# Kernel tuning notes

Hardware: AMD Instinct MI355X
Metric: run time of the kernel (lower is better)

Reference implementation:

```python
import jax, jax.numpy as jnp
import numpy as np

B, S, CIN = 4, 512, 512
H, I, N, R, K, L = 768, 1536, 16, 48, 4, 4  # mamba-130m dims, 4 layers
EPS = 1e-5


def setup_inputs() -> dict:
    key = jax.random.key(0)
    ks = jax.random.split(key, 8)
    g = lambda k, shape, s=0.02: jax.random.normal(k, shape, jnp.float32) * s
    x = jax.random.normal(ks[0], (B, S, CIN), jnp.float32)
    # HF Mamba init: A = 1..N repeated over channels, stored as log
    A_log = jnp.log(jnp.broadcast_to(jnp.arange(1, N + 1, dtype=jnp.float32), (L, I, N)))
    dt_bias = jnp.full((L, I), float(np.log(np.expm1(0.01))), jnp.float32)  # softplus^-1(0.01)
    return {
        'x': x,
        'W_in': g(ks[1], (CIN, H)), 'b_in': jnp.zeros((H,), jnp.float32),
        'norm_w': jnp.ones((L, H), jnp.float32),
        'in_proj_w': g(ks[2], (L, H, 2 * I)),
        'conv_w': g(ks[3], (L, I, K), 0.2), 'conv_b': jnp.zeros((L, I), jnp.float32),
        'x_proj_w': g(ks[4], (L, I, R + 2 * N)),
        'dt_proj_w': g(ks[5], (L, R, I), 0.05), 'dt_proj_b': dt_bias,
        'A_log': A_log, 'D': jnp.ones((L, I), jnp.float32),
        'out_proj_w': g(ks[6], (L, I, H)),
        'norm_f_w': jnp.ones((H,), jnp.float32),
    }


def _rmsnorm(x, w):
    return x * jax.lax.rsqrt(jnp.mean(x * x, -1, keepdims=True) + EPS) * w


def _selective_scan(xc, dt, A, Bm, Cm, Dp):
    # xc, dt: [B,S,I]; A: [I,N]; Bm, Cm: [B,S,N]; Dp: [I]
    dA = jnp.exp(dt[..., None] * A)                    # [B,S,I,N]
    dBx = (dt * xc)[..., None] * Bm[:, :, None, :]     # [B,S,I,N]

    def step(h, ins):
        dA_t, dBx_t, C_t = ins
        h = dA_t * h + dBx_t                           # [B,I,N]
        return h, jnp.einsum('bin,bn->bi', h, C_t)

    h0 = jnp.zeros((xc.shape[0], I, N), xc.dtype)
    _, ys = jax.lax.scan(step, h0, (jnp.swapaxes(dA, 0, 1),
                                    jnp.swapaxes(dBx, 0, 1),
                                    jnp.swapaxes(Cm, 0, 1)))
    return jnp.swapaxes(ys, 0, 1) + xc * Dp            # [B,S,I]


def _block(h, nw, ipw, cw, cb, xpw, dpw, dpb, Al, Dp, opw):
    res = h
    u = _rmsnorm(h, nw)
    xz = u @ ipw                                       # [B,S,2I]
    xc, z = jnp.split(xz, 2, axis=-1)
    xc_t = jnp.swapaxes(xc, 1, 2)                      # [B,I,S]
    xc_t = jax.lax.conv_general_dilated(
        xc_t, cw[:, None, :], (1,), [(K - 1, 0)],
        dimension_numbers=('NCH', 'OIH', 'NCH'), feature_group_count=I)
    xc = jax.nn.silu(jnp.swapaxes(xc_t, 1, 2) + cb)    # causal depthwise conv + SiLU
    dbc = xc @ xpw                                     # [B,S,R+2N]
    dt, Bm, Cm = dbc[..., :R], dbc[..., R:R + N], dbc[..., R + N:]
    dt = jax.nn.softplus(dt @ dpw + dpb)               # [B,S,I]
    y = _selective_scan(xc, dt, -jnp.exp(Al), Bm, Cm, Dp)
    y = y * jax.nn.silu(z)
    return res + y @ opw


def reference(x, W_in, b_in, norm_w, in_proj_w, conv_w, conv_b, x_proj_w,
              dt_proj_w, dt_proj_b, A_log, D, out_proj_w, norm_f_w):
    h = x @ W_in + b_in                                # project_in
    for l in range(L):
        h = _block(h, norm_w[l], in_proj_w[l], conv_w[l], conv_b[l], x_proj_w[l],
                   dt_proj_w[l], dt_proj_b[l], A_log[l], D[l], out_proj_w[l])
    return _rmsnorm(h, norm_f_w)                       # final norm_f; dropout = identity (eval)
```

## Files before the change

kernel.cpp:

```cpp
#include <hip/hip_runtime.h>
#include <cmath>

#define B_    4
#define S_    512
#define CIN_  512
#define H_    768
#define I_    1536
#define N_    16
#define R_    48
#define K_    4
#define L_    4
#define EPS_  1e-5f
#define MROWS (B_ * S_)
#define C_    16
#define T_    (S_ / C_)

typedef __attribute__((ext_vector_type(8))) short bf16x8;
typedef __attribute__((ext_vector_type(4))) float f32x4;
typedef __attribute__((ext_vector_type(4))) short s16x4;

__device__ __forceinline__ float fexpf(float x) { return __expf(x); }
__device__ __forceinline__ float siluf(float x) { return x / (1.f + __expf(-x)); }
__device__ __forceinline__ float softplusf(float x) { return x > 20.f ? x : __logf(1.f + __expf(x)); }
__device__ __forceinline__ short f2bf(float f) {
    union { float f; unsigned u; } v; v.f = f;
    unsigned r = v.u + 0x7fff + ((v.u >> 16) & 1);
    return (short)(r >> 16);
}
__device__ __forceinline__ float bf2f(short s) {
    union { float f; unsigned u; } v;
    v.u = ((unsigned)(unsigned short)s) << 16;
    return v.f;
}

#define GLOAD16(g, l) __builtin_amdgcn_global_load_lds( \
    (const __attribute__((address_space(1))) void*)(g), \
    (__attribute__((address_space(3))) void*)(l), 16, 0, 0)

#define ASTRIDE (64 * 64)
#define BSTRIDE (128 * 64)

__global__ __launch_bounds__(256) void gemm_mfma(
    const short* __restrict__ A, const short* __restrict__ Bt,
    const float* __restrict__ bias, void* __restrict__ Cv_,
    int M, int N, int Kd, int lda, int ldb, int ldc, int ep)
{
    __shared__ __align__(16) short Asl[2 * ASTRIDE];
    __shared__ __align__(16) short Bsl[2 * BSTRIDE];
    const int tid = threadIdx.x;
    const int ln  = tid & 63;
    const int wv  = tid >> 6;
    const int wm  = wv >> 1, wn = wv & 1;
    const int nwg  = gridDim.x * gridDim.y;
    const int orig = blockIdx.y * gridDim.x + blockIdx.x;
    const int qq   = nwg >> 3;
    const int swz  = (orig & 7) * qq + (orig >> 3);
    const int bx   = swz % gridDim.x;
    const int by   = swz / gridDim.x;
    const int row0 = by * 64;
    const int col0 = bx * 128;
    const int nz   = gridDim.z;
    const int kchunk = Kd / nz;
    const int kbeg   = blockIdx.z * kchunk;
    float* C = (float*)Cv_;
    short* Cb = (short*)Cv_;

    f32x4 acc[2][4];
    #pragma unroll
    for (int i = 0; i < 2; ++i)
        #pragma unroll
        for (int j = 0; j < 4; ++j) acc[i][j] = (f32x4){0.f, 0.f, 0.f, 0.f};

    const int ca0 = tid, ca1 = tid + 256;
    const int rowa0 = ca0 >> 3, kpa0 = (ca0 & 7) ^ (rowa0 & 7);
    const int rowa1 = ca1 >> 3, kpa1 = (ca1 & 7) ^ (rowa1 & 7);
    const short* ga0 = A + (size_t)(row0 + rowa0) * lda + kpa0 * 8;
    const short* ga1 = A + (size_t)(row0 + rowa1) * lda + kpa1 * 8;
    const int cb0 = tid, cb1 = tid + 256, cb2 = tid + 512, cb3 = tid + 768;
    const int rowb0 = cb0 >> 3, kpb0 = (cb0 & 7) ^ (rowb0 & 7);
    const int rowb1 = cb1 >> 3, kpb1 = (cb1 & 7) ^ (rowb1 & 7);
    const int rowb2 = cb2 >> 3, kpb2 = (cb2 & 7) ^ (rowb2 & 7);
    const int rowb3 = cb3 >> 3, kpb3 = (cb3 & 7) ^ (rowb3 & 7);
    const short* gb0 = Bt + (size_t)(col0 + rowb0) * ldb + kpb0 * 8;
    const short* gb1 = Bt + (size_t)(col0 + rowb1) * ldb + kpb1 * 8;
    const short* gb2 = Bt + (size_t)(col0 + rowb2) * ldb + kpb2 * 8;
    const short* gb3 = Bt + (size_t)(col0 + rowb3) * ldb + kpb3 * 8;
    short* la0 = &Asl[(wv * 64) * 8];
    short* la1 = &Asl[(256 + wv * 64) * 8];
    short* lb0 = &Bsl[(wv * 64) * 8];
    short* lb1 = &Bsl[(256 + wv * 64) * 8];
    short* lb2 = &Bsl[(512 + wv * 64) * 8];
    short* lb3 = &Bsl[(768 + wv * 64) * 8];

    const int lrow = ln & 15;
    const int kq0  = ln >> 4;
    const int nt   = kchunk / 64;

#define ISSUE_TILE(T, BI) do {                      \
    const int kI_ = kbeg + (T) * 64;                \
    GLOAD16(ga0 + kI_, la0 + (BI) * ASTRIDE);       \
    GLOAD16(ga1 + kI_, la1 + (BI) * ASTRIDE);       \
    GLOAD16(gb0 + kI_, lb0 + (BI) * BSTRIDE);       \
    GLOAD16(gb1 + kI_, lb1 + (BI) * BSTRIDE);       \
    GLOAD16(gb2 + kI_, lb2 + (BI) * BSTRIDE);       \
    GLOAD16(gb3 + kI_, lb3 + (BI) * BSTRIDE);       \
} while (0)

    ISSUE_TILE(0, 0);
    __syncthreads();

    for (int t = 0; t < nt; ++t) {
        const int cur = t & 1;
        const int nxt = cur ^ 1;
        if (t + 1 < nt) ISSUE_TILE(t + 1, nxt);
        const short* Ac = &Asl[cur * ASTRIDE];
        const short* Bc = &Bsl[cur * BSTRIDE];
        #pragma unroll
        for (int kk = 0; kk < 2; ++kk) {
            const int kq = kk * 4 + kq0;
            bf16x8 af[2], bfr[4];
            #pragma unroll
            for (int fm = 0; fm < 2; ++fm) {
                int r = wm * 32 + fm * 16 + lrow;
                int slot = r * 8 + (kq ^ (r & 7));
                af[fm] = *(const bf16x8*)&Ac[slot * 8];
            }
            #pragma unroll
            for (int fn = 0; fn < 4; ++fn) {
                int r = wn * 64 + fn * 16 + lrow;
                int slot = r * 8 + (kq ^ (r & 7));
                bfr[fn] = *(const bf16x8*)&Bc[slot * 8];
            }
            #pragma unroll
            for (int fm = 0; fm < 2; ++fm)
                #pragma unroll
                for (int fn = 0; fn < 4; ++fn)
                    acc[fm][fn] = __builtin_amdgcn_mfma_f32_16x16x32_bf16(
                        af[fm], bfr[fn], acc[fm][fn], 0, 0, 0);
        }
        __syncthreads();
    }
#undef ISSUE_TILE

    const int erow = (ln >> 4) * 4;
    const int ecol = ln & 15;
    const size_t zoff = (size_t)blockIdx.z * M * ldc;
    #pragma unroll
    for (int fm = 0; fm < 2; ++fm) {
        #pragma unroll
        for (int fn = 0; fn < 4; ++fn) {
            int gn = col0 + wn * 64 + fn * 16 + ecol;
            if (gn >= N) continue;
            #pragma unroll
            for (int r = 0; r < 4; ++r) {
                int gm = row0 + wm * 32 + fm * 16 + erow + r;
                float v = acc[fm][fn][r];
                size_t o = (size_t)gm * ldc + gn;
                if (nz > 1) { C[zoff + o] = v; continue; }
                if (ep == 4)      { Cb[o] = f2bf(v); continue; }
                if (ep == 5)      { Cb[o] = f2bf(softplusf(v + bias[gn])); continue; }
                if (ep == 1)      v += bias[gn];
                else if (ep == 2) v  = softplusf(v + bias[gn]);
                else if (ep == 3) v += C[o];
                C[o] = v;
            }
        }
    }
}

__global__ __launch_bounds__(256) void reduce_parts(
    const float* __restrict__ part, float* __restrict__ C,
    const float* __restrict__ bias, short* __restrict__ d48,
    int total, int ldc, int nz, int mode)
{
    int idx = blockIdx.x * 256 + threadIdx.x;
    if (idx >= total) return;
    size_t strideZ = (size_t)total;
    float s = 0.f;
    for (int z = 0; z < nz; ++z) s += part[idx + z * strideZ];
    if (mode == 1)      s += bias[idx % ldc];
    else if (mode == 2) s += C[idx];
    C[idx] = s;
    if (d48) {
        int row = idx / ldc, col = idx - row * ldc;
        if (col < 48)       d48[(size_t)row * 64 + col] = f2bf(s);
        else if (col >= 64) d48[(size_t)row * 64 + (col - 16)] = 0;
    }
}

__global__ __launch_bounds__(256) void reduce_h_rms(
    const float* __restrict__ part, float* __restrict__ h,
    const float* __restrict__ bias, const float* __restrict__ w,
    short* __restrict__ ubf, float* __restrict__ outf, int nz, int mode)
{
    const int row = blockIdx.x;
    const int t   = threadIdx.x;
    const size_t base = (size_t)row * H_;
    const size_t strideZ = (size_t)MROWS * H_;
    float v0, v1, v2;
    {
        size_t i0 = base + t, i1 = i0 + 256, i2 = i0 + 512;
        float s0 = 0.f, s1 = 0.f, s2 = 0.f;
        for (int z = 0; z < nz; ++z) {
            size_t zo = (size_t)z * strideZ;
            s0 += part[i0 + zo]; s1 += part[i1 + zo]; s2 += part[i2 + zo];
        }
        if (mode == 0) {
            s0 += bias[t]; s1 += bias[t + 256]; s2 += bias[t + 512];
        } else {
            s0 += h[i0]; s1 += h[i1]; s2 += h[i2];
        }
        h[i0] = s0; h[i1] = s1; h[i2] = s2;
        v0 = s0; v1 = s1; v2 = s2;
    }
    float ss = v0 * v0 + v1 * v1 + v2 * v2;
    #pragma unroll
    for (int off = 32; off > 0; off >>= 1) ss += __shfl_down(ss, off, 64);
    __shared__ float red[4];
    __shared__ float stot;
    if ((t & 63) == 0) red[t >> 6] = ss;
    __syncthreads();
    if (t == 0) stot = red[0] + red[1] + red[2] + red[3];
    __syncthreads();
    const float scale = rsqrtf(stot / (float)H_ + EPS_);
    if (mode == 2) {
        outf[base + t]       = v0 * scale * w[t];
        outf[base + t + 256] = v1 * scale * w[t + 256];
        outf[base + t + 512] = v2 * scale * w[t + 512];
    } else {
        ubf[base + t]       = f2bf(v0 * scale * w[t]);
        ubf[base + t + 256] = f2bf(v1 * scale * w[t + 256]);
        ubf[base + t + 512] = f2bf(v2 * scale * w[t + 512]);
    }
}

__global__ __launch_bounds__(256) void wtrans(
    const float* __restrict__ in0, short* __restrict__ out0,
    int Kd, int Nn, int Kpad, int Npad, size_t inStride, size_t outStride)
{
    const float* in  = in0  + blockIdx.z * inStride;
    short*       out = out0 + blockIdx.z * outStride;
    __shared__ float t[32][33];
    const int n0 = blockIdx.x * 32, k0 = blockIdx.y * 32;
    const int tx = threadIdx.x, ty = threadIdx.y;
    #pragma unroll
    for (int j = 0; j < 32; j += 8) {
        int k = k0 + ty + j, n = n0 + tx;
        t[ty + j][tx] = (k < Kd && n < Nn) ? in[(size_t)k * Nn + n] : 0.f;
    }
    __syncthreads();
    #pragma unroll
    for (int j = 0; j < 32; j += 8) {
        int np = n0 + ty + j, kp = k0 + tx;
        if (np < Npad && kp < Kpad) out[(size_t)np * Kpad + kp] = f2bf(t[tx][ty + j]);
    }
}

__global__ __launch_bounds__(256) void cast_bf16(
    const float* __restrict__ in, short* __restrict__ out, int n4)
{
    int i = blockIdx.x * 256 + threadIdx.x;
    if (i >= n4) return;
    float4 v = ((const float4*)in)[i];
    out[i * 4 + 0] = f2bf(v.x); out[i * 4 + 1] = f2bf(v.y);
    out[i * 4 + 2] = f2bf(v.z); out[i * 4 + 3] = f2bf(v.w);
}

__global__ __launch_bounds__(256) void conv_silu_kernel(
    const short* __restrict__ xzbf, const float* __restrict__ cw,
    const float* __restrict__ cb, short* __restrict__ xcb16)
{
    int idx = blockIdx.x * 256 + threadIdx.x;
    if (idx >= (MROWS / 4) * (I_ / 4)) return;
    const int i4 = (idx % (I_ / 4)) * 4;
    const int g4 = idx / (I_ / 4);
    const int s0 = (g4 % (S_ / 4)) * 4;
    const int b  = g4 / (S_ / 4);
    const short* base = xzbf + (size_t)b * S_ * (2 * I_) + i4;

    float4 wch[4];
    #pragma unroll
    for (int c = 0; c < 4; ++c) wch[c] = *(const float4*)&cw[(i4 + c) * K_];
    const float4 bv = *(const float4*)&cb[i4];

    float xv[7][4];
    #pragma unroll
    for (int r = 0; r < 7; ++r) {
        int row = s0 - 3 + r;
        if (row >= 0) {
            s16x4 t = *(const s16x4*)&base[(size_t)row * (2 * I_)];
            xv[r][0] = bf2f(t[0]); xv[r][1] = bf2f(t[1]);
            xv[r][2] = bf2f(t[2]); xv[r][3] = bf2f(t[3]);
        } else {
            xv[r][0] = 0.f; xv[r][1] = 0.f; xv[r][2] = 0.f; xv[r][3] = 0.f;
        }
    }

    #pragma unroll
    for (int j = 0; j < 4; ++j) {
        float a0 = bv.x, a1 = bv.y, a2 = bv.z, a3 = bv.w;
        #pragma unroll
        for (int k = 0; k < K_; ++k) {
            const float w0 = ((const float*)&wch[0])[k];
            const float w1 = ((const float*)&wch[1])[k];
            const float w2 = ((const float*)&wch[2])[k];
            const float w3 = ((const float*)&wch[3])[k];
            a0 = fmaf(w0, xv[j + k][0], a0);
            a1 = fmaf(w1, xv[j + k][1], a1);
            a2 = fmaf(w2, xv[j + k][2], a2);
            a3 = fmaf(w3, xv[j + k][3], a3);
        }
        s16x4 r;
        r[0] = f2bf(siluf(a0)); r[1] = f2bf(siluf(a1));
        r[2] = f2bf(siluf(a2)); r[3] = f2bf(siluf(a3));
        *(s16x4*)&xcb16[((size_t)b * S_ + s0 + j) * I_ + i4] = r;
    }
}

__global__ __launch_bounds__(256) void scan_pass1(
    const short* __restrict__ xcbf, const short* __restrict__ dtbf,
    const float* __restrict__ dbc, const float* __restrict__ A_log,
    short* __restrict__ P, short* __restrict__ hend)
{
    __shared__ float Bsh[T_][16];
    __shared__ float dtsh[T_][64];
    __shared__ float xcsh[T_][64];
    const int tid = threadIdx.x;
    const int lc  = tid >> 2;
    const int sub = tid & 3;
    const int ib  = blockIdx.x % (I_ / 64);
    const int c   = (blockIdx.x / (I_ / 64)) % C_;
    const int b   = blockIdx.x / ((I_ / 64) * C_);
    const int i   = ib * 64 + lc;
    const int s0  = c * T_;

    for (int idx = tid; idx < T_ * 4; idx += 256) {
        int row = idx >> 2, q = idx & 3;
        *(float4*)&Bsh[row][q * 4] =
            *(const float4*)&dbc[((size_t)b * S_ + s0 + row) * 80 + R_ + q * 4];
    }
    for (int idx = tid; idx < T_ * 16; idx += 256) {
        int row = idx >> 4, q = idx & 15;
        size_t g = ((size_t)b * S_ + s0 + row) * I_ + ib * 64 + q * 4;
        s16x4 dv = *(const s16x4*)&dtbf[g];
        dtsh[row][q * 4 + 0] = bf2f(dv[0]);
        dtsh[row][q * 4 + 1] = bf2f(dv[1]);
        dtsh[row][q * 4 + 2] = bf2f(dv[2]);
        dtsh[row][q * 4 + 3] = bf2f(dv[3]);
        s16x4 xv = *(const s16x4*)&xcbf[g];
        xcsh[row][q * 4 + 0] = bf2f(xv[0]);
        xcsh[row][q * 4 + 1] = bf2f(xv[1]);
        xcsh[row][q * 4 + 2] = bf2f(xv[2]);
        xcsh[row][q * 4 + 3] = bf2f(xv[3]);
    }

    float4 al = *(const float4*)&A_log[i * N_ + sub * 4];
    float a[4] = {-fexpf(al.x), -fexpf(al.y), -fexpf(al.z), -fexpf(al.w)};
    float h[4] = {0.f, 0.f, 0.f, 0.f}, p[4] = {1.f, 1.f, 1.f, 1.f};
    __syncthreads();

    #pragma unroll 4
    for (int s = 0; s < T_; ++s) {
        float dtv = dtsh[s][lc];
        float xcv = xcsh[s][lc];
        float4 Bv = *(const float4*)&Bsh[s][sub * 4];
        float dx = dtv * xcv;
        #pragma unroll
        for (int j = 0; j < 4; ++j) {
            float dA = fexpf(dtv * a[j]);
            float Bj = (j == 0) ? Bv.x : (j == 1) ? Bv.y : (j == 2) ? Bv.z : Bv.w;
            h[j] = fmaf(dA, h[j], dx * Bj);
            p[j] *= dA;
        }
    }
    size_t o = (((size_t)b * C_ + c) * I_ + i) * N_ + sub * 4;
    s16x4 pv, hv;
    pv[0] = f2bf(p[0]); pv[1] = f2bf(p[1]); pv[2] = f2bf(p[2]); pv[3] = f2bf(p[3]);
    hv[0] = f2bf(h[0]); hv[1] = f2bf(h[1]); hv[2] = f2bf(h[2]); hv[3] = f2bf(h[3]);
    *(s16x4*)&P[o]    = pv;
    *(s16x4*)&hend[o] = hv;
}

__global__ __launch_bounds__(256) void scan_pass2(
    const short* __restrict__ P, const short* __restrict__ hend,
    short* __restrict__ Hstart)
{
    int idx = blockIdx.x * 256 + threadIdx.x;
    if (idx >= B_ * I_ * N_) return;
    int n = idx & 15;
    int i = (idx >> 4) % I_;
    int b = idx / (I_ * N_);
    float H = 0.f;
    #pragma unroll
    for (int c = 0; c < C_; ++c) {
        size_t o = (((size_t)b * C_ + c) * I_ + i) * (size_t)N_ + n;
        Hstart[o] = f2bf(H);
        H = fmaf(bf2f(P[o]), H, bf2f(hend[o]));
    }
}

__global__ __launch_bounds__(256) void scan_pass3(
    const short* __restrict__ xcbf, const short* __restrict__ dtbf,
    const float* __restrict__ dbc, const short* __restrict__ xzbf,
    const float* __restrict__ A_log, const float* __restrict__ D,
    const short* __restrict__ Hstart, short* __restrict__ y16)
{
    __shared__ float Bsh[T_][16];
    __shared__ float Csh[T_][16];
    __shared__ float dtsh[T_][64];
    __shared__ float xcsh[T_][64];
    __shared__ float zsh[T_][64];
    __shared__ short ysh[T_][64];
    const int tid = threadIdx.x;
    const int lc  = tid >> 2;
    const int sub = tid & 3;
    const int ib  = blockIdx.x % (I_ / 64);
    const int c   = (blockIdx.x / (I_ / 64)) % C_;
    const int b   = blockIdx.x / ((I_ / 64) * C_);
    const int i   = ib * 64 + lc;
    const int s0  = c * T_;

    for (int idx = tid; idx < T_ * 4; idx += 256) {
        int row = idx >> 2, q = idx & 3;
        const float* src = &dbc[((size_t)b * S_ + s0 + row) * 80 + R_];
        *(float4*)&Bsh[row][q * 4] = *(const float4*)&src[q * 4];
        *(float4*)&Csh[row][q * 4] = *(const float4*)&src[16 + q * 4];
    }
    for (int idx = tid; idx < T_ * 16; idx += 256) {
        int row = idx >> 4, q = idx & 15;
        size_t g = ((size_t)b * S_ + s0 + row) * I_ + ib * 64 + q * 4;
        s16x4 dv = *(const s16x4*)&dtbf[g];
        dtsh[row][q * 4 + 0] = bf2f(dv[0]);
        dtsh[row][q * 4 + 1] = bf2f(dv[1]);
        dtsh[row][q * 4 + 2] = bf2f(dv[2]);
        dtsh[row][q * 4 + 3] = bf2f(dv[3]);
        s16x4 xv = *(const s16x4*)&xcbf[g];
        xcsh[row][q * 4 + 0] = bf2f(xv[0]);
        xcsh[row][q * 4 + 1] = bf2f(xv[1]);
        xcsh[row][q * 4 + 2] = bf2f(xv[2]);
        xcsh[row][q * 4 + 3] = bf2f(xv[3]);
        size_t gz = ((size_t)b * S_ + s0 + row) * (2 * I_) + I_ + ib * 64 + q * 4;
        s16x4 zv = *(const s16x4*)&xzbf[gz];
        zsh[row][q * 4 + 0] = bf2f(zv[0]);
        zsh[row][q * 4 + 1] = bf2f(zv[1]);
        zsh[row][q * 4 + 2] = bf2f(zv[2]);
        zsh[row][q * 4 + 3] = bf2f(zv[3]);
    }

    float4 al = *(const float4*)&A_log[i * N_ + sub * 4];
    float a[4] = {-fexpf(al.x), -fexpf(al.y), -fexpf(al.z), -fexpf(al.w)};
    const float Dv = D[i];

    size_t ho = (((size_t)b * C_ + c) * I_ + i) * N_ + sub * 4;
    s16x4 h0 = *(const s16x4*)&Hstart[ho];
    float h[4] = {bf2f(h0[0]), bf2f(h0[1]), bf2f(h0[2]), bf2f(h0[3])};
    __syncthreads();

    #pragma unroll 4
    for (int s = 0; s < T_; ++s) {
        float dtv = dtsh[s][lc];
        float xcv = xcsh[s][lc];
        float4 Bv = *(const float4*)&Bsh[s][sub * 4];
        float4 Cv = *(const float4*)&Csh[s][sub * 4];
        float dx = dtv * xcv;
        float yv;
        {
            float dA0 = fexpf(dtv * a[0]);
            float dA1 = fexpf(dtv * a[1]);
            float dA2 = fexpf(dtv * a[2]);
            float dA3 = fexpf(dtv * a[3]);
            h[0] = fmaf(dA0, h[0], dx * Bv.x);
            h[1] = fmaf(dA1, h[1], dx * Bv.y);
            h[2] = fmaf(dA2, h[2], dx * Bv.z);
            h[3] = fmaf(dA3, h[3], dx * Bv.w);
            yv = h[0] * Cv.x;
            yv = fmaf(h[1], Cv.y, yv);
            yv = fmaf(h[2], Cv.z, yv);
            yv = fmaf(h[3], Cv.w, yv);
        }
        yv += __shfl_xor(yv, 1, 4);
        yv += __shfl_xor(yv, 2, 4);
        if (sub == 0) {
            float zv = zsh[s][lc];
            ysh[s][lc] = f2bf((yv + xcv * Dv) * siluf(zv));
        }
    }
    __syncthreads();
    for (int idx = tid; idx < T_ * 16; idx += 256) {
        int row = idx >> 4, q = idx & 15;
        size_t g = ((size_t)b * S_ + s0 + row) * I_ + ib * 64 + q * 4;
        *(s16x4*)&y16[g] = *(const s16x4*)&ysh[row][q * 4];
    }
}

extern "C" void kernel_launch(void* const* d_in, const int* in_sizes, int n_in,
                              void* d_out, int out_size, void* d_ws, size_t ws_size,
                              hipStream_t stream)
{
    const float* x     = (const float*)d_in[0];
    const float* W_in  = (const float*)d_in[1];
    const float* b_in  = (const float*)d_in[2];
    const float* norm_w= (const float*)d_in[3];
    const float* ipw   = (const float*)d_in[4];
    const float* cw    = (const float*)d_in[5];
    const float* cb    = (const float*)d_in[6];
    const float* xpw   = (const float*)d_in[7];
    const float* dpw   = (const float*)d_in[8];
    const float* dpb   = (const float*)d_in[9];
    const float* A_log = (const float*)d_in[10];
    const float* Dp    = (const float*)d_in[11];
    const float* opw   = (const float*)d_in[12];
    const float* nfw   = (const float*)d_in[13];
    float* out = (float*)d_out;

    float* wsf  = (float*)d_ws;
    float* h    = wsf;  wsf += (size_t)MROWS * H_;
    float* parts= wsf;  wsf += (size_t)3 * MROWS * H_;
    float* dbcb = wsf;  wsf += (size_t)MROWS * 80;
    short* wss   = (short*)wsf;
    short* x_bf  = wss;  wss += (size_t)MROWS * CIN_;
    short* u_bf  = wss;  wss += (size_t)MROWS * H_;
    short* xz_bf = wss;  wss += (size_t)MROWS * 2 * I_;
    short* xc_bf = wss;  wss += (size_t)MROWS * I_;
    short* dt_bf = wss;  wss += (size_t)MROWS * I_;
    short* y_bf  = wss;  wss += (size_t)MROWS * I_;
    short* dbc48 = wss;  wss += (size_t)MROWS * 64;
    short* Pb    = wss;  wss += (size_t)B_ * C_ * I_ * N_;
    short* heb   = wss;  wss += (size_t)B_ * C_ * I_ * N_;
    short* Hsb   = wss;  wss += (size_t)B_ * C_ * I_ * N_;
    short* WinT  = wss;  wss += (size_t)H_ * CIN_;
    short* ipwT  = wss;  wss += (size_t)L_ * 2 * I_ * H_;
    short* xpwT  = wss;  wss += (size_t)L_ * 128 * I_;
    short* opwT  = wss;  wss += (size_t)L_ * H_ * I_;
    short* dpwT  = wss;  wss += (size_t)L_ * I_ * 64;

    float* part_x = parts;

    const dim3 blk(256);
    const dim3 tblk(32, 8);

    cast_bf16<<<(MROWS * CIN_ / 4 + 255) / 256, blk, 0, stream>>>(x, x_bf, MROWS * CIN_ / 4);
    wtrans<<<dim3(H_ / 32, CIN_ / 32, 1), tblk, 0, stream>>>(
        W_in, WinT, CIN_, H_, CIN_, H_, 0, 0);
    wtrans<<<dim3(2 * I_ / 32, H_ / 32, L_), tblk, 0, stream>>>(
        ipw, ipwT, H_, 2 * I_, H_, 2 * I_, (size_t)H_ * 2 * I_, (size_t)2 * I_ * H_);
    wtrans<<<dim3(128 / 32, I_ / 32, L_), tblk, 0, stream>>>(
        xpw, xpwT, I_, 80, I_, 128, (size_t)I_ * 80, (size_t)128 * I_);
    wtrans<<<dim3(H_ / 32, I_ / 32, L_), tblk, 0, stream>>>(
        opw, opwT, I_, H_, I_, H_, (size_t)I_ * H_, (size_t)H_ * I_);
    wtrans<<<dim3(I_ / 32, 64 / 32, L_), tblk, 0, stream>>>(
        dpw, dpwT, R_, I_, 64, I_, (size_t)R_ * I_, (size_t)I_ * 64);

    gemm_mfma<<<dim3(H_ / 128, MROWS / 64, 2), blk, 0, stream>>>(
        x_bf, WinT, nullptr, parts, MROWS, H_, CIN_, CIN_, CIN_, H_, 0);
    reduce_h_rms<<<MROWS, blk, 0, stream>>>(
        parts, h, b_in, norm_w, u_bf, nullptr, 2, 0);

    const int scan_blocks = B_ * C_ * (I_ / 64);
    const int conv_blocks = ((MROWS / 4) * (I_ / 4) + 255) / 256;

    for (int l = 0; l < L_; ++l) {
        gemm_mfma<<<dim3(2 * I_ / 128, MROWS / 64, 1), blk, 0, stream>>>(
            u_bf, ipwT + (size_t)l * 2 * I_ * H_, nullptr, xz_bf,
            MROWS, 2 * I_, H_, H_, H_, 2 * I_, 4);
        conv_silu_kernel<<<conv_blocks, blk, 0, stream>>>(
            xz_bf, cw + l * I_ * K_, cb + l * I_, xc_bf);
        gemm_mfma<<<dim3(1, MROWS / 64, 8), blk, 0, stream>>>(
            xc_bf, xpwT + (size_t)l * 128 * I_, nullptr, part_x,
            MROWS, 80, I_, I_, I_, 80, 0);
        reduce_parts<<<(MROWS * 80 + 255) / 256, blk, 0, stream>>>(
            part_x, dbcb, nullptr, dbc48, MROWS * 80, 80, 8, 0);
        gemm_mfma<<<dim3(I_ / 128, MROWS / 64, 1), blk, 0, stream>>>(
            dbc48, dpwT + (size_t)l * I_ * 64, dpb + (size_t)l * I_, dt_bf,
            MROWS, I_, 64, 64, 64, I_, 5);
        scan_pass1<<<scan_blocks, blk, 0, stream>>>(
            xc_bf, dt_bf, dbcb, A_log + l * I_ * N_, Pb, heb);
        scan_pass2<<<(B_ * I_ * N_ + 255) / 256, blk, 0, stream>>>(Pb, heb, Hsb);
        scan_pass3<<<scan_blocks, blk, 0, stream>>>(
            xc_bf, dt_bf, dbcb, xz_bf, A_log + l * I_ * N_, Dp + l * I_, Hsb, y_bf);
        gemm_mfma<<<dim3(H_ / 128, MROWS / 64, 3), blk, 0, stream>>>(
            y_bf, opwT + (size_t)l * H_ * I_, nullptr, parts,
            MROWS, H_, I_, I_, I_, H_, 0);
        if (l < L_ - 1) {
            reduce_h_rms<<<MROWS, blk, 0, stream>>>(
                parts, h, nullptr, norm_w + (l + 1) * H_, u_bf, nullptr, 3, 1);
        } else {
            reduce_h_rms<<<MROWS, blk, 0, stream>>>(
                parts, h, nullptr, nfw, nullptr, out, 3, 2);
        }
    }
}
```

Before: 476.0 us.

## Fold chunk-prefix pass into scan pass 3 and skip last chunk in pass 1

Removes the separate scan_pass2 kernel. Each pass-3 block now recomputes its own starting state by serially combining the P/hend summaries of all preceding chunks. Pass 1 also skips the last chunk, whose summary is never consumed. This saves one kernel launch per layer, the Hstart buffer round trip, and 1/16 of pass-1 work. In exchange, later chunks do redundant serial reads of up to 15 prior summaries per thread.

```diff
diff --git a/kernel.cpp b/kernel.cpp
--- a/kernel.cpp
+++ b/kernel.cpp
@@ -329,8 +329,9 @@
     const int lc  = tid >> 2;
     const int sub = tid & 3;
     const int ib  = blockIdx.x % (I_ / 64);
-    const int c   = (blockIdx.x / (I_ / 64)) % C_;
-    const int b   = blockIdx.x / ((I_ / 64) * C_);
+    const int rest= blockIdx.x / (I_ / 64);
+    const int c   = rest % (C_ - 1);
+    const int b   = rest / (C_ - 1);
     const int i   = ib * 64 + lc;
     const int s0  = c * T_;
 
@@ -381,29 +382,12 @@
     *(s16x4*)&hend[o] = hv;
 }
 
-__global__ __launch_bounds__(256) void scan_pass2(
-    const short* __restrict__ P, const short* __restrict__ hend,
-    short* __restrict__ Hstart)
-{
-    int idx = blockIdx.x * 256 + threadIdx.x;
-    if (idx >= B_ * I_ * N_) return;
-    int n = idx & 15;
-    int i = (idx >> 4) % I_;
-    int b = idx / (I_ * N_);
-    float H = 0.f;
-    #pragma unroll
-    for (int c = 0; c < C_; ++c) {
-        size_t o = (((size_t)b * C_ + c) * I_ + i) * (size_t)N_ + n;
-        Hstart[o] = f2bf(H);
-        H = fmaf(bf2f(P[o]), H, bf2f(hend[o]));
-    }
-}
-
 __global__ __launch_bounds__(256) void scan_pass3(
     const short* __restrict__ xcbf, const short* __restrict__ dtbf,
     const float* __restrict__ dbc, const short* __restrict__ xzbf,
     const float* __restrict__ A_log, const float* __restrict__ D,
-    const short* __restrict__ Hstart, short* __restrict__ y16)
+    const short* __restrict__ P, const short* __restrict__ hend,
+    short* __restrict__ y16)
 {
     __shared__ float Bsh[T_][16];
     __shared__ float Csh[T_][16];
@@ -451,9 +435,16 @@
     float a[4] = {-fexpf(al.x), -fexpf(al.y), -fexpf(al.z), -fexpf(al.w)};
     const float Dv = D[i];
 
-    size_t ho = (((size_t)b * C_ + c) * I_ + i) * N_ + sub * 4;
-    s16x4 h0 = *(const s16x4*)&Hstart[ho];
-    float h[4] = {bf2f(h0[0]), bf2f(h0[1]), bf2f(h0[2]), bf2f(h0[3])};
+    float h[4] = {0.f, 0.f, 0.f, 0.f};
+    for (int j = 0; j < c; ++j) {
+        size_t o = (((size_t)b * C_ + j) * I_ + i) * N_ + sub * 4;
+        s16x4 pv = *(const s16x4*)&P[o];
+        s16x4 hv = *(const s16x4*)&hend[o];
+        h[0] = fmaf(bf2f(pv[0]), h[0], bf2f(hv[0]));
+        h[1] = fmaf(bf2f(pv[1]), h[1], bf2f(hv[1]));
+        h[2] = fmaf(bf2f(pv[2]), h[2], bf2f(hv[2]));
+        h[3] = fmaf(bf2f(pv[3]), h[3], bf2f(hv[3]));
+    }
     __syncthreads();
 
     #pragma unroll 4
@@ -527,7 +518,6 @@
     short* dbc48 = wss;  wss += (size_t)MROWS * 64;
     short* Pb    = wss;  wss += (size_t)B_ * C_ * I_ * N_;
     short* heb   = wss;  wss += (size_t)B_ * C_ * I_ * N_;
-    short* Hsb   = wss;  wss += (size_t)B_ * C_ * I_ * N_;
     short* WinT  = wss;  wss += (size_t)H_ * CIN_;
     short* ipwT  = wss;  wss += (size_t)L_ * 2 * I_ * H_;
     short* xpwT  = wss;  wss += (size_t)L_ * 128 * I_;
@@ -556,7 +546,8 @@
     reduce_h_rms<<<MROWS, blk, 0, stream>>>(
         parts, h, b_in, norm_w, u_bf, nullptr, 2, 0);
 
-    const int scan_blocks = B_ * C_ * (I_ / 64);
+    const int scan1_blocks = B_ * (C_ - 1) * (I_ / 64);
+    const int scan3_blocks = B_ * C_ * (I_ / 64);
     const int conv_blocks = ((MROWS / 4) * (I_ / 4) + 255) / 256;
 
     for (int l = 0; l < L_; ++l) {
@@ -573,11 +564,11 @@
         gemm_mfma<<<dim3(I_ / 128, MROWS / 64, 1), blk, 0, stream>>>(
             dbc48, dpwT + (size_t)l * I_ * 64, dpb + (size_t)l * I_, dt_bf,
             MROWS, I_, 64, 64, 64, I_, 5);
-        scan_pass1<<<scan_blocks, blk, 0, stream>>>(
+        scan_pass1<<<scan1_blocks, blk, 0, stream>>>(
             xc_bf, dt_bf, dbcb, A_log + l * I_ * N_, Pb, heb);
-        scan_pass2<<<(B_ * I_ * N_ + 255) / 256, blk, 0, stream>>>(Pb, heb, Hsb);
-        scan_pass3<<<scan_blocks, blk, 0, stream>>>(
-            xc_bf, dt_bf, dbcb, xz_bf, A_log + l * I_ * N_, Dp + l * I_, Hsb, y_bf);
+        scan_pass3<<<scan3_blocks, blk, 0, stream>>>(
+            xc_bf, dt_bf, dbcb, xz_bf, A_log + l * I_ * N_, Dp + l * I_,
+            Pb, heb, y_bf);
         gemm_mfma<<<dim3(H_ / 128, MROWS / 64, 3), blk, 0, stream>>>(
             y_bf, opwT + (size_t)l * H_ * I_, nullptr, parts,
             MROWS, H_, I_, I_, I_, H_, 0);
```

New measurement: 491.4 us. +3.2%, slower.
